# Kernel tuning notes

Measured on AMD Instinct MI355X. Metric: run time of the kernel, lower is better.

## Reference

```python
import jax, jax.numpy as jnp
import numpy as np
import math

D_HEAD = 64
D_MODEL = 1024
N_HEADS = D_MODEL // D_HEAD
MAX_TOKENS = 2048
BATCH = 4
SEQ = 2048


def setup_inputs() -> dict:
    key = jax.random.key(0)
    k1, k2, k3, k4, k5 = jax.random.split(key, 5)
    residual_stream = jax.random.normal(k1, (BATCH, SEQ, D_MODEL), dtype=jnp.float32)
    # kaiming_normal_ (fan_in = d_model for [head, d_model, d_head] with default mode)
    std_qkv = math.sqrt(2.0 / D_MODEL)
    weight_query = jax.random.normal(k2, (N_HEADS, D_MODEL, D_HEAD), dtype=jnp.float32) * std_qkv
    weight_key = jax.random.normal(k3, (N_HEADS, D_MODEL, D_HEAD), dtype=jnp.float32) * std_qkv
    weight_value = jax.random.normal(k4, (N_HEADS, D_MODEL, D_HEAD), dtype=jnp.float32) * std_qkv
    # xavier_normal_ for [d_model, d_model]
    std_out = math.sqrt(2.0 / (D_MODEL + D_MODEL))
    weight_out = jax.random.normal(k5, (D_MODEL, D_MODEL), dtype=jnp.float32) * std_out
    return {
        "residual_stream": residual_stream,
        "weight_query": weight_query,
        "weight_key": weight_key,
        "weight_value": weight_value,
        "weight_out": weight_out,
    }


def reference(residual_stream, weight_query, weight_key, weight_value, weight_out):
    # residual_stream: [b, s, m]; weights: [h, m, d]
    q = jnp.einsum("bsm,hmd->bhsd", residual_stream, weight_query)
    k = jnp.einsum("bsm,hmd->bhsd", residual_stream, weight_key)
    v = jnp.einsum("bsm,hmd->bhsd", residual_stream, weight_value)
    scores = jnp.einsum("bhqd,bhkd->bhqk", q, k) / math.sqrt(D_HEAD)  # [b,h,s,s]
    n = scores.shape[-1]
    causal = jnp.tril(jnp.ones((n, n), dtype=bool))
    scores = jnp.where(causal, scores, -jnp.inf)
    attn = jax.nn.softmax(scores, axis=-1)
    out = jnp.einsum("bhqk,bhkd->bhqd", attn, v)  # [b,h,s,d]
    b, h, s, d = out.shape
    concat = out.transpose(0, 2, 1, 3).reshape(b, s, h * d)  # [b,s,m]
    return jnp.einsum("bsm,mn->bsn", concat, weight_out)
```

## Files before the change

kernel.cpp:

```cpp
#include <hip/hip_runtime.h>
#include <hip/hip_bf16.h>
#include <math.h>

#define BATCH 4
#define SEQ   2048
#define DM    1024
#define NH    16
#define DH    64

#define QSCALE 0.1803368801111204f

typedef __bf16 bf16x8 __attribute__((ext_vector_type(8)));
typedef __bf16 bf16x4 __attribute__((ext_vector_type(4)));
typedef float  f32x4  __attribute__((ext_vector_type(4)));

typedef const __attribute__((address_space(1))) unsigned int guint;
typedef __attribute__((address_space(3)))       unsigned int luint;

__device__ __forceinline__ void async16(const __bf16* g, __bf16* l) {
    __builtin_amdgcn_global_load_lds((guint*)g, (luint*)l, 16, 0, 0);
}

__device__ __forceinline__ float fast_exp2(float x) {
#if __has_builtin(__builtin_amdgcn_exp2f)
    return __builtin_amdgcn_exp2f(x);
#else
    float r; asm("v_exp_f32 %0, %1" : "=v"(r) : "v"(x)); return r;
#endif
}
__device__ __forceinline__ float fast_rcp(float x) {
#if __has_builtin(__builtin_amdgcn_rcpf)
    return __builtin_amdgcn_rcpf(x);
#else
    float r; asm("v_rcp_f32 %0, %1" : "=v"(r) : "v"(x)); return r;
#endif
}

__device__ __forceinline__ bf16x8 load8f(const float* __restrict__ base, size_t idx) {
    const float4 a = *(const float4*)(base + idx);
    const float4 b = *(const float4*)(base + idx + 4);
    bf16x8 r;
    r[0] = (__bf16)a.x; r[1] = (__bf16)a.y; r[2] = (__bf16)a.z; r[3] = (__bf16)a.w;
    r[4] = (__bf16)b.x; r[5] = (__bf16)b.y; r[6] = (__bf16)b.z; r[7] = (__bf16)b.w;
    return r;
}

__global__ __launch_bounds__(256)
void prep_kernel(const float* __restrict__ X,
                 const float* __restrict__ Wq,
                 const float* __restrict__ Wk,
                 const float* __restrict__ Wv,
                 const float* __restrict__ Wo,
                 __bf16* __restrict__ Xb,
                 __bf16* __restrict__ Wqt,
                 __bf16* __restrict__ Wkt,
                 __bf16* __restrict__ Wvt,
                 __bf16* __restrict__ Wot)
{
    __shared__ __bf16 T[64][65];
    const int t  = threadIdx.x;
    const int bx = blockIdx.x;

    if (bx < 4096) {
        size_t idx = ((size_t)bx * 256 + t) * 8;
        *(bf16x8*)&Xb[idx] = load8f(X, idx);
        return;
    }

    const float* src;
    __bf16* dst;
    int k0, n0, srcN;
    if (bx < 4096 + 768) {
        const int i = bx - 4096;
        const int z = i >> 4;
        const int m = z >> 4;
        const int h = z & 15;
        src  = (m == 0 ? Wq : m == 1 ? Wk : Wv) + (size_t)h * DM * DH;
        dst  = (m == 0 ? Wqt : m == 1 ? Wkt : Wvt) + (size_t)h * DH * DM;
        k0   = (i & 15) * 64;
        n0   = 0;
        srcN = DH;
    } else {
        const int i = bx - 4096 - 768;
        src  = Wo;
        dst  = Wot;
        k0   = (i & 15) * 64;
        n0   = (i >> 4) * 64;
        srcN = DM;
    }

#pragma unroll
    for (int i = 0; i < 4; ++i) {
        int row = i * 16 + (t >> 4);
        int col = (t & 15) * 4;
        float4 v = *(const float4*)&src[(size_t)(k0 + row) * srcN + n0 + col];
        T[col + 0][row] = (__bf16)v.x;
        T[col + 1][row] = (__bf16)v.y;
        T[col + 2][row] = (__bf16)v.z;
        T[col + 3][row] = (__bf16)v.w;
    }
    __syncthreads();
#pragma unroll
    for (int i = 0; i < 4; ++i) {
        int n  = i * 16 + (t >> 4);
        int kc = (t & 15) * 4;
        bf16x4 v;
        v[0] = T[n][kc + 0]; v[1] = T[n][kc + 1];
        v[2] = T[n][kc + 2]; v[3] = T[n][kc + 3];
        *(bf16x4*)&dst[(size_t)(n0 + n) * DM + k0 + kc] = v;
    }
}

__global__ __launch_bounds__(256)
void qkv_kernel(const __bf16* __restrict__ Xb,
                const __bf16* __restrict__ Wqt,
                const __bf16* __restrict__ Wkt,
                const __bf16* __restrict__ Wvt,
                __bf16* __restrict__ Qo,
                __bf16* __restrict__ Ko,
                __bf16* __restrict__ Vto)
{
    const int rowTile = blockIdx.x;
    const int h       = blockIdx.y;
    const size_t woff = (size_t)h * DH * DM;

    __shared__ __align__(16) __bf16 As[128 * 32];
    __shared__ __align__(16) __bf16 Bq[64 * 32];
    __shared__ __align__(16) __bf16 Bk[64 * 32];
    __shared__ __align__(16) __bf16 Bv[64 * 32];

    const int t    = threadIdx.x;
    const int wave = t >> 6;
    const int lane = t & 63;
    const int l15  = lane & 15;
    const int quad = lane >> 4;

    f32x4 aq[2][4], ak[2][4], av[2][4];
#pragma unroll
    for (int s = 0; s < 2; ++s)
#pragma unroll
        for (int i = 0; i < 4; ++i) {
            aq[s][i] = (f32x4){0.f, 0.f, 0.f, 0.f};
            ak[s][i] = (f32x4){0.f, 0.f, 0.f, 0.f};
            av[s][i] = (f32x4){0.f, 0.f, 0.f, 0.f};
        }

    const int r0 = rowTile * 128;
    const int lrow = lane >> 2;
    const int lcol = (lane & 3) * 8;

    for (int k0 = 0; k0 < DM; k0 += 32) {
        __syncthreads();
#pragma unroll
        for (int c = 0; c < 2; ++c) {
            const int rb = wave * 32 + c * 16;
            async16(&Xb[(size_t)(r0 + rb + lrow) * DM + k0 + lcol], &As[rb * 32]);
        }
        {
            const int rb = wave * 16;
            async16(&Wqt[woff + (size_t)(rb + lrow) * DM + k0 + lcol], &Bq[rb * 32]);
            async16(&Wkt[woff + (size_t)(rb + lrow) * DM + k0 + lcol], &Bk[rb * 32]);
            async16(&Wvt[woff + (size_t)(rb + lrow) * DM + k0 + lcol], &Bv[rb * 32]);
        }
        __syncthreads();

        bf16x8 a0 = *(const bf16x8*)&As[(wave * 16 + l15) * 32 + quad * 8];
        bf16x8 a1 = *(const bf16x8*)&As[(64 + wave * 16 + l15) * 32 + quad * 8];
#pragma unroll
        for (int ct = 0; ct < 4; ++ct) {
            bf16x8 bq = *(const bf16x8*)&Bq[(ct * 16 + l15) * 32 + quad * 8];
            aq[0][ct] = __builtin_amdgcn_mfma_f32_16x16x32_bf16(a0, bq, aq[0][ct], 0, 0, 0);
            aq[1][ct] = __builtin_amdgcn_mfma_f32_16x16x32_bf16(a1, bq, aq[1][ct], 0, 0, 0);
            bf16x8 bk = *(const bf16x8*)&Bk[(ct * 16 + l15) * 32 + quad * 8];
            ak[0][ct] = __builtin_amdgcn_mfma_f32_16x16x32_bf16(a0, bk, ak[0][ct], 0, 0, 0);
            ak[1][ct] = __builtin_amdgcn_mfma_f32_16x16x32_bf16(a1, bk, ak[1][ct], 0, 0, 0);
            bf16x8 bv = *(const bf16x8*)&Bv[(ct * 16 + l15) * 32 + quad * 8];
            av[0][ct] = __builtin_amdgcn_mfma_f32_16x16x32_bf16(a0, bv, av[0][ct], 0, 0, 0);
            av[1][ct] = __builtin_amdgcn_mfma_f32_16x16x32_bf16(a1, bv, av[1][ct], 0, 0, 0);
        }
    }

#pragma unroll
    for (int st = 0; st < 2; ++st) {
        const int rbase = r0 + st * 64 + wave * 16 + quad * 4;
        const int b = rbase >> 11;
        const int s = rbase & (SEQ - 1);
        const size_t bh = (size_t)(b * NH + h);
#pragma unroll
        for (int ct = 0; ct < 4; ++ct) {
            const int d = ct * 16 + l15;
#pragma unroll
            for (int reg = 0; reg < 4; ++reg) {
                Qo[(bh * SEQ + s + reg) * DH + d] = (__bf16)(aq[st][ct][reg] * QSCALE);
                Ko[(bh * SEQ + s + reg) * DH + d] = (__bf16)ak[st][ct][reg];
            }
            bf16x4 vv;
            vv[0] = (__bf16)av[st][ct][0]; vv[1] = (__bf16)av[st][ct][1];
            vv[2] = (__bf16)av[st][ct][2]; vv[3] = (__bf16)av[st][ct][3];
            *(bf16x4*)&Vto[(bh * DH + d) * SEQ + s] = vv;
        }
    }
}

__global__ __launch_bounds__(256)
void attn_kernel(const __bf16* __restrict__ Q,
                 const __bf16* __restrict__ K,
                 const __bf16* __restrict__ Vt,
                 __bf16* __restrict__ Cat)
{
    const int x   = blockIdx.x;
    const int qtA = x;
    const int qtB = 31 - x;
    const int bh  = blockIdx.y;
    const int b   = bh >> 4;
    const int h   = bh & 15;

    const __bf16* Qg  = Q  + (size_t)bh * SEQ * DH;
    const __bf16* Kg  = K  + (size_t)bh * SEQ * DH;
    const __bf16* Vtg = Vt + (size_t)bh * DH * SEQ;

    __shared__ __align__(16) __bf16 Ks[64 * 72];
    __shared__ __align__(16) __bf16 Vs[64 * 72];
    __shared__ __align__(16) __bf16 Ps[64 * 72];

    const int t    = threadIdx.x;
    const int wave = t >> 6;
    const int lane = t & 63;
    const int l15  = lane & 15;
    const int quad = lane >> 4;

    bf16x8 qfA[2], qfB[2];
    {
        const size_t rA = (size_t)(qtA * 64 + wave * 16 + l15);
        qfA[0] = *(const bf16x8*)&Qg[rA * DH + quad * 8];
        qfA[1] = *(const bf16x8*)&Qg[rA * DH + 32 + quad * 8];
        const size_t rB = (size_t)(qtB * 64 + wave * 16 + l15);
        qfB[0] = *(const bf16x8*)&Qg[rB * DH + quad * 8];
        qfB[1] = *(const bf16x8*)&Qg[rB * DH + 32 + quad * 8];
    }

    bf16x8 ones;
#pragma unroll
    for (int j = 0; j < 8; ++j) ones[j] = (__bf16)1.0f;

    f32x4 oA[4], oB[4], olA, olB;
#pragma unroll
    for (int ct = 0; ct < 4; ++ct) {
        oA[ct] = (f32x4){0.f, 0.f, 0.f, 0.f};
        oB[ct] = (f32x4){0.f, 0.f, 0.f, 0.f};
    }
    olA = (f32x4){0.f, 0.f, 0.f, 0.f};
    olB = (f32x4){0.f, 0.f, 0.f, 0.f};

    const int srow0 = t >> 3;
    const int scol  = (t & 7) * 8;
    bf16x8 kreg[2], vreg[2];
#pragma unroll
    for (int i = 0; i < 2; ++i) {
        int row = srow0 + i * 32;
        kreg[i] = *(const bf16x8*)&Kg[(size_t)row * DH + scol];
        vreg[i] = *(const bf16x8*)&Vtg[(size_t)row * SEQ + scol];
    }

    auto half_step = [&](const bf16x8* qf, f32x4* o, f32x4& ol, bool diag) {
        f32x4 sc[4];
#pragma unroll
        for (int ct = 0; ct < 4; ++ct) {
            sc[ct] = (f32x4){0.f, 0.f, 0.f, 0.f};
            bf16x8 b0 = *(const bf16x8*)&Ks[(ct * 16 + l15) * 72 + quad * 8];
            sc[ct] = __builtin_amdgcn_mfma_f32_16x16x32_bf16(qf[0], b0, sc[ct], 0, 0, 0);
            bf16x8 b1 = *(const bf16x8*)&Ks[(ct * 16 + l15) * 72 + 32 + quad * 8];
            sc[ct] = __builtin_amdgcn_mfma_f32_16x16x32_bf16(qf[1], b1, sc[ct], 0, 0, 0);
        }
        if (diag) {
#pragma unroll
            for (int ct = 0; ct < 4; ++ct)
#pragma unroll
                for (int r = 0; r < 4; ++r) {
                    int qr = wave * 16 + quad * 4 + r;
                    int kc = ct * 16 + l15;
                    if (kc > qr) sc[ct][r] = -INFINITY;
                }
        }
#pragma unroll
        for (int ct = 0; ct < 4; ++ct)
#pragma unroll
            for (int r = 0; r < 4; ++r)
                sc[ct][r] = fast_exp2(sc[ct][r]);

#pragma unroll
        for (int ct = 0; ct < 4; ++ct)
#pragma unroll
            for (int r = 0; r < 4; ++r)
                Ps[(wave * 16 + quad * 4 + r) * 72 + ct * 16 + l15] =
                    (__bf16)sc[ct][r];

        bf16x8 af0 = *(const bf16x8*)&Ps[(wave * 16 + l15) * 72 + quad * 8];
        bf16x8 af1 = *(const bf16x8*)&Ps[(wave * 16 + l15) * 72 + 32 + quad * 8];

#pragma unroll
        for (int ct = 0; ct < 4; ++ct) {
            bf16x8 v0 = *(const bf16x8*)&Vs[(ct * 16 + l15) * 72 + quad * 8];
            o[ct] = __builtin_amdgcn_mfma_f32_16x16x32_bf16(af0, v0, o[ct], 0, 0, 0);
            bf16x8 v1 = *(const bf16x8*)&Vs[(ct * 16 + l15) * 72 + 32 + quad * 8];
            o[ct] = __builtin_amdgcn_mfma_f32_16x16x32_bf16(af1, v1, o[ct], 0, 0, 0);
        }
        ol = __builtin_amdgcn_mfma_f32_16x16x32_bf16(af0, ones, ol, 0, 0, 0);
        ol = __builtin_amdgcn_mfma_f32_16x16x32_bf16(af1, ones, ol, 0, 0, 0);
    };

    for (int kt = 0; kt <= qtB; ++kt) {
        __syncthreads();
#pragma unroll
        for (int i = 0; i < 2; ++i) {
            int row = srow0 + i * 32;
            *(bf16x8*)&Ks[row * 72 + scol] = kreg[i];
            *(bf16x8*)&Vs[row * 72 + scol] = vreg[i];
        }
        __syncthreads();

        {
            const int kvn = (kt < qtB ? kt + 1 : kt) * 64;
#pragma unroll
            for (int i = 0; i < 2; ++i) {
                int row = srow0 + i * 32;
                kreg[i] = *(const bf16x8*)&Kg[(size_t)(kvn + row) * DH + scol];
                vreg[i] = *(const bf16x8*)&Vtg[(size_t)row * SEQ + kvn + scol];
            }
        }

        half_step(qfB, oB, olB, kt == qtB);
        if (kt <= qtA)
            half_step(qfA, oA, olA, kt == qtA);
    }

#pragma unroll
    for (int ct = 0; ct < 4; ++ct)
#pragma unroll
        for (int r = 0; r < 4; ++r) {
            int rr = wave * 16 + quad * 4 + r;
            int sA = qtA * 64 + rr;
            int sB = qtB * 64 + rr;
            Cat[((size_t)(b * SEQ + sA)) * DM + h * DH + ct * 16 + l15] =
                (__bf16)(oA[ct][r] * fast_rcp(olA[r]));
            Cat[((size_t)(b * SEQ + sB)) * DM + h * DH + ct * 16 + l15] =
                (__bf16)(oB[ct][r] * fast_rcp(olB[r]));
        }
}

__global__ __launch_bounds__(256)
void oproj_kernel(const __bf16* __restrict__ A,
                  const __bf16* __restrict__ Wot,
                  float* __restrict__ C)
{
    const int rowTile = blockIdx.x;
    const int colTile = blockIdx.y;
    const int r0 = rowTile * 128;
    const int n0 = colTile * 128;

    __shared__ __align__(16) __bf16 As[128 * 32];
    __shared__ __align__(16) __bf16 Bs[128 * 32];

    const int t    = threadIdx.x;
    const int wave = t >> 6;
    const int lane = t & 63;
    const int l15  = lane & 15;
    const int quad = lane >> 4;

    f32x4 acc[2][8];
#pragma unroll
    for (int s = 0; s < 2; ++s)
#pragma unroll
        for (int i = 0; i < 8; ++i) acc[s][i] = (f32x4){0.f, 0.f, 0.f, 0.f};

    const int lrow = lane >> 2;
    const int lcol = (lane & 3) * 8;

    for (int k0 = 0; k0 < DM; k0 += 32) {
        __syncthreads();
#pragma unroll
        for (int c = 0; c < 2; ++c) {
            const int rb = wave * 32 + c * 16;
            async16(&A  [(size_t)(r0 + rb + lrow) * DM + k0 + lcol], &As[rb * 32]);
            async16(&Wot[(size_t)(n0 + rb + lrow) * DM + k0 + lcol], &Bs[rb * 32]);
        }
        __syncthreads();

        bf16x8 a0 = *(const bf16x8*)&As[(wave * 16 + l15) * 32 + quad * 8];
        bf16x8 a1 = *(const bf16x8*)&As[(64 + wave * 16 + l15) * 32 + quad * 8];
#pragma unroll
        for (int ct = 0; ct < 8; ++ct) {
            bf16x8 bb = *(const bf16x8*)&Bs[(ct * 16 + l15) * 32 + quad * 8];
            acc[0][ct] = __builtin_amdgcn_mfma_f32_16x16x32_bf16(a0, bb, acc[0][ct], 0, 0, 0);
            acc[1][ct] = __builtin_amdgcn_mfma_f32_16x16x32_bf16(a1, bb, acc[1][ct], 0, 0, 0);
        }
    }

#pragma unroll
    for (int st = 0; st < 2; ++st)
#pragma unroll
        for (int ct = 0; ct < 8; ++ct)
#pragma unroll
            for (int reg = 0; reg < 4; ++reg) {
                int r = r0 + st * 64 + wave * 16 + quad * 4 + reg;
                int n = n0 + ct * 16 + l15;
                C[(size_t)r * DM + n] = acc[st][ct][reg];
            }
}

extern "C" void kernel_launch(void* const* d_in, const int* in_sizes, int n_in,
                              void* d_out, int out_size, void* d_ws, size_t ws_size,
                              hipStream_t stream)
{
    (void)in_sizes; (void)n_in; (void)out_size; (void)ws_size;
    const float* X  = (const float*)d_in[0];
    const float* Wq = (const float*)d_in[1];
    const float* Wk = (const float*)d_in[2];
    const float* Wv = (const float*)d_in[3];
    const float* Wo = (const float*)d_in[4];
    float* out = (float*)d_out;

    char* ws = (char*)d_ws;
    const size_t wqkv_b = (size_t)NH * DM * DH * sizeof(__bf16);
    const size_t wo_b   = (size_t)DM * DM * sizeof(__bf16);
    const size_t big_b  = (size_t)BATCH * NH * SEQ * DH * sizeof(__bf16);
    __bf16* Wqt = (__bf16*)(ws);
    __bf16* Wkt = (__bf16*)(ws + wqkv_b);
    __bf16* Wvt = (__bf16*)(ws + 2 * wqkv_b);
    __bf16* Wot = (__bf16*)(ws + 3 * wqkv_b);
    __bf16* Qb  = (__bf16*)(ws + 3 * wqkv_b + wo_b);
    __bf16* Kb  = (__bf16*)(ws + 3 * wqkv_b + wo_b + big_b);
    __bf16* Vtb = (__bf16*)(ws + 3 * wqkv_b + wo_b + 2 * big_b);
    __bf16* Cat = (__bf16*)(ws + 3 * wqkv_b + wo_b + 3 * big_b);
    __bf16* Xb  = (__bf16*)(ws + 3 * wqkv_b + wo_b + 4 * big_b);

    prep_kernel<<<dim3(4096 + 768 + 256), 256, 0, stream>>>(
        X, Wq, Wk, Wv, Wo, Xb, Wqt, Wkt, Wvt, Wot);
    qkv_kernel<<<dim3(64, 16), 256, 0, stream>>>(Xb, Wqt, Wkt, Wvt, Qb, Kb, Vtb);
    attn_kernel<<<dim3(16, 64), 256, 0, stream>>>(Qb, Kb, Vtb, Cat);
    oproj_kernel<<<dim3(64, 8), 256, 0, stream>>>(Cat, Wot, out);
}
```

Measured before the change: 274.0 us.

## Restructure QKV projection as one concatenated GEMM with 128x128 tiles; add setprio around MFMAs

The per-head QKV kernel, which used 64-column tiles for each of Q, K and V, is replaced by a single GEMM over a concatenated weight of 3072 output columns. It uses 128x128 tiles on a 64x24 grid and routes each column tile to the Q, K or transposed-V output in the epilogue. The change relies on Wqt, Wkt and Wvt being laid out contiguously in the workspace, which they are. The attention kernel also raises wave priority around its MFMA blocks to favour matrix issue over other waves. This should improve the shape of the B-tile loads and the grid balance, but each block now has 64 accumulator registers.

```diff
diff --git a/kernel.cpp b/kernel.cpp
--- a/kernel.cpp
+++ b/kernel.cpp
@@ -112,22 +112,19 @@
 }
 
 __global__ __launch_bounds__(256)
-void qkv_kernel(const __bf16* __restrict__ Xb,
-                const __bf16* __restrict__ Wqt,
-                const __bf16* __restrict__ Wkt,
-                const __bf16* __restrict__ Wvt,
-                __bf16* __restrict__ Qo,
-                __bf16* __restrict__ Ko,
-                __bf16* __restrict__ Vto)
+void qkv_gemm(const __bf16* __restrict__ Xb,
+              const __bf16* __restrict__ Wcat,
+              __bf16* __restrict__ Qo,
+              __bf16* __restrict__ Ko,
+              __bf16* __restrict__ Vto)
 {
     const int rowTile = blockIdx.x;
-    const int h       = blockIdx.y;
-    const size_t woff = (size_t)h * DH * DM;
+    const int colTile = blockIdx.y;
+    const int r0 = rowTile * 128;
+    const int n0 = colTile * 128;
 
     __shared__ __align__(16) __bf16 As[128 * 32];
-    __shared__ __align__(16) __bf16 Bq[64 * 32];
-    __shared__ __align__(16) __bf16 Bk[64 * 32];
-    __shared__ __align__(16) __bf16 Bv[64 * 32];
+    __shared__ __align__(16) __bf16 Bs[128 * 32];
 
     const int t    = threadIdx.x;
     const int wave = t >> 6;
@@ -135,17 +132,12 @@
     const int l15  = lane & 15;
     const int quad = lane >> 4;
 
-    f32x4 aq[2][4], ak[2][4], av[2][4];
+    f32x4 acc[2][8];
 #pragma unroll
     for (int s = 0; s < 2; ++s)
 #pragma unroll
-        for (int i = 0; i < 4; ++i) {
-            aq[s][i] = (f32x4){0.f, 0.f, 0.f, 0.f};
-            ak[s][i] = (f32x4){0.f, 0.f, 0.f, 0.f};
-            av[s][i] = (f32x4){0.f, 0.f, 0.f, 0.f};
-        }
-
-    const int r0 = rowTile * 128;
+        for (int i = 0; i < 8; ++i) acc[s][i] = (f32x4){0.f, 0.f, 0.f, 0.f};
+
     const int lrow = lane >> 2;
     const int lcol = (lane & 3) * 8;
 
@@ -154,50 +146,57 @@
 #pragma unroll
         for (int c = 0; c < 2; ++c) {
             const int rb = wave * 32 + c * 16;
-            async16(&Xb[(size_t)(r0 + rb + lrow) * DM + k0 + lcol], &As[rb * 32]);
-        }
-        {
-            const int rb = wave * 16;
-            async16(&Wqt[woff + (size_t)(rb + lrow) * DM + k0 + lcol], &Bq[rb * 32]);
-            async16(&Wkt[woff + (size_t)(rb + lrow) * DM + k0 + lcol], &Bk[rb * 32]);
-            async16(&Wvt[woff + (size_t)(rb + lrow) * DM + k0 + lcol], &Bv[rb * 32]);
+            async16(&Xb  [(size_t)(r0 + rb + lrow) * DM + k0 + lcol], &As[rb * 32]);
+            async16(&Wcat[(size_t)(n0 + rb + lrow) * DM + k0 + lcol], &Bs[rb * 32]);
         }
         __syncthreads();
 
         bf16x8 a0 = *(const bf16x8*)&As[(wave * 16 + l15) * 32 + quad * 8];
         bf16x8 a1 = *(const bf16x8*)&As[(64 + wave * 16 + l15) * 32 + quad * 8];
 #pragma unroll
-        for (int ct = 0; ct < 4; ++ct) {
-            bf16x8 bq = *(const bf16x8*)&Bq[(ct * 16 + l15) * 32 + quad * 8];
-            aq[0][ct] = __builtin_amdgcn_mfma_f32_16x16x32_bf16(a0, bq, aq[0][ct], 0, 0, 0);
-            aq[1][ct] = __builtin_amdgcn_mfma_f32_16x16x32_bf16(a1, bq, aq[1][ct], 0, 0, 0);
-            bf16x8 bk = *(const bf16x8*)&Bk[(ct * 16 + l15) * 32 + quad * 8];
-            ak[0][ct] = __builtin_amdgcn_mfma_f32_16x16x32_bf16(a0, bk, ak[0][ct], 0, 0, 0);
-            ak[1][ct] = __builtin_amdgcn_mfma_f32_16x16x32_bf16(a1, bk, ak[1][ct], 0, 0, 0);
-            bf16x8 bv = *(const bf16x8*)&Bv[(ct * 16 + l15) * 32 + quad * 8];
-            av[0][ct] = __builtin_amdgcn_mfma_f32_16x16x32_bf16(a0, bv, av[0][ct], 0, 0, 0);
-            av[1][ct] = __builtin_amdgcn_mfma_f32_16x16x32_bf16(a1, bv, av[1][ct], 0, 0, 0);
-        }
-    }
-
-#pragma unroll
-    for (int st = 0; st < 2; ++st) {
-        const int rbase = r0 + st * 64 + wave * 16 + quad * 4;
-        const int b = rbase >> 11;
-        const int s = rbase & (SEQ - 1);
-        const size_t bh = (size_t)(b * NH + h);
-#pragma unroll
-        for (int ct = 0; ct < 4; ++ct) {
-            const int d = ct * 16 + l15;
-#pragma unroll
-            for (int reg = 0; reg < 4; ++reg) {
-                Qo[(bh * SEQ + s + reg) * DH + d] = (__bf16)(aq[st][ct][reg] * QSCALE);
-                Ko[(bh * SEQ + s + reg) * DH + d] = (__bf16)ak[st][ct][reg];
+        for (int ct = 0; ct < 8; ++ct) {
+            bf16x8 bb = *(const bf16x8*)&Bs[(ct * 16 + l15) * 32 + quad * 8];
+            acc[0][ct] = __builtin_amdgcn_mfma_f32_16x16x32_bf16(a0, bb, acc[0][ct], 0, 0, 0);
+            acc[1][ct] = __builtin_amdgcn_mfma_f32_16x16x32_bf16(a1, bb, acc[1][ct], 0, 0, 0);
+        }
+    }
+
+    const int mat = colTile >> 3;
+    if (mat < 2) {
+        __bf16* __restrict__ Dst = (mat == 0) ? Qo : Ko;
+        const float scale = (mat == 0) ? QSCALE : 1.0f;
+#pragma unroll
+        for (int st = 0; st < 2; ++st) {
+            const int r = r0 + st * 64 + wave * 16 + quad * 4;
+            const int b = r >> 11;
+            const int s = r & (SEQ - 1);
+#pragma unroll
+            for (int ct = 0; ct < 8; ++ct) {
+                const int n = (n0 + ct * 16 + l15) & 1023;
+                const int h = n >> 6;
+                const int d = n & 63;
+                const size_t base = (((size_t)(b * NH + h)) * SEQ + s) * DH + d;
+#pragma unroll
+                for (int reg = 0; reg < 4; ++reg)
+                    Dst[base + (size_t)reg * DH] = (__bf16)(acc[st][ct][reg] * scale);
             }
-            bf16x4 vv;
-            vv[0] = (__bf16)av[st][ct][0]; vv[1] = (__bf16)av[st][ct][1];
-            vv[2] = (__bf16)av[st][ct][2]; vv[3] = (__bf16)av[st][ct][3];
-            *(bf16x4*)&Vto[(bh * DH + d) * SEQ + s] = vv;
+        }
+    } else {
+#pragma unroll
+        for (int st = 0; st < 2; ++st) {
+            const int r = r0 + st * 64 + wave * 16 + quad * 4;
+            const int b = r >> 11;
+            const int s = r & (SEQ - 1);
+#pragma unroll
+            for (int ct = 0; ct < 8; ++ct) {
+                const int n = (n0 + ct * 16 + l15) & 1023;
+                const int h = n >> 6;
+                const int d = n & 63;
+                bf16x4 vv;
+                vv[0] = (__bf16)acc[st][ct][0]; vv[1] = (__bf16)acc[st][ct][1];
+                vv[2] = (__bf16)acc[st][ct][2]; vv[3] = (__bf16)acc[st][ct][3];
+                *(bf16x4*)&Vto[(((size_t)(b * NH + h)) * DH + d) * SEQ + s] = vv;
+            }
         }
     }
 }
@@ -264,6 +263,7 @@
 
     auto half_step = [&](const bf16x8* qf, f32x4* o, f32x4& ol, bool diag) {
         f32x4 sc[4];
+        __builtin_amdgcn_s_setprio(1);
 #pragma unroll
         for (int ct = 0; ct < 4; ++ct) {
             sc[ct] = (f32x4){0.f, 0.f, 0.f, 0.f};
@@ -272,6 +272,7 @@
             bf16x8 b1 = *(const bf16x8*)&Ks[(ct * 16 + l15) * 72 + 32 + quad * 8];
             sc[ct] = __builtin_amdgcn_mfma_f32_16x16x32_bf16(qf[1], b1, sc[ct], 0, 0, 0);
         }
+        __builtin_amdgcn_s_setprio(0);
         if (diag) {
 #pragma unroll
             for (int ct = 0; ct < 4; ++ct)
@@ -298,6 +299,7 @@
         bf16x8 af0 = *(const bf16x8*)&Ps[(wave * 16 + l15) * 72 + quad * 8];
         bf16x8 af1 = *(const bf16x8*)&Ps[(wave * 16 + l15) * 72 + 32 + quad * 8];
 
+        __builtin_amdgcn_s_setprio(1);
 #pragma unroll
         for (int ct = 0; ct < 4; ++ct) {
             bf16x8 v0 = *(const bf16x8*)&Vs[(ct * 16 + l15) * 72 + quad * 8];
@@ -307,6 +309,7 @@
         }
         ol = __builtin_amdgcn_mfma_f32_16x16x32_bf16(af0, ones, ol, 0, 0, 0);
         ol = __builtin_amdgcn_mfma_f32_16x16x32_bf16(af1, ones, ol, 0, 0, 0);
+        __builtin_amdgcn_s_setprio(0);
     };
 
     for (int kt = 0; kt <= qtB; ++kt) {
@@ -436,7 +439,7 @@
 
     prep_kernel<<<dim3(4096 + 768 + 256), 256, 0, stream>>>(
         X, Wq, Wk, Wv, Wo, Xb, Wqt, Wkt, Wvt, Wot);
-    qkv_kernel<<<dim3(64, 16), 256, 0, stream>>>(Xb, Wqt, Wkt, Wvt, Qb, Kb, Vtb);
+    qkv_gemm<<<dim3(64, 24), 256, 0, stream>>>(Xb, Wqt, Qb, Kb, Vtb);
     attn_kernel<<<dim3(16, 64), 256, 0, stream>>>(Qb, Kb, Vtb, Cat);
     oproj_kernel<<<dim3(64, 8), 256, 0, stream>>>(Cat, Wot, out);
 }
```

Measured after the change: 263.5 us. 1.04x faster.
